# Performance work log

Measured on AMD Instinct MI355X. Metric: run time of the kernel, lower is better.

Reference implementation:

```python
import jax, jax.numpy as jnp
import numpy as np

BATCH, INPUT_SIZE, NUM_UNITS = 64, 256, 768
UNFOLDS = 6

def setup_inputs() -> dict:
    key = jax.random.key(0)
    ks = jax.random.split(key, 12)
    F, H = INPUT_SIZE, NUM_UNITS
    inputs = jax.random.normal(ks[0], (BATCH, F), dtype=jnp.float32)
    state = jax.random.normal(ks[1], (BATCH, H), dtype=jnp.float32)
    sensory_mu = jax.random.uniform(ks[2], (F, H), dtype=jnp.float32) * 0.5 + 0.3
    sensory_sigma = jax.random.uniform(ks[3], (F, H), dtype=jnp.float32) * 5.0 + 3.0
    sensory_W = jax.random.uniform(ks[4], (F, H), dtype=jnp.float32, minval=0.01, maxval=1.0)
    sensory_erev = (2.0 * jax.random.randint(ks[5], (F, H), 0, 2) - 1.0).astype(jnp.float32)
    mu = jax.random.uniform(ks[6], (H, H), dtype=jnp.float32) * 0.5 + 0.3
    sigma = jax.random.uniform(ks[7], (H, H), dtype=jnp.float32) * 5.0 + 3.0
    W = jax.random.uniform(ks[8], (H, H), dtype=jnp.float32, minval=0.01, maxval=1.0)
    erev = (2.0 * jax.random.randint(ks[9], (H, H), 0, 2) - 1.0).astype(jnp.float32)
    vleak = jax.random.uniform(ks[10], (H,), dtype=jnp.float32) * 0.4 - 0.2
    gleak = jnp.ones((H,), dtype=jnp.float32)          # gleak_init_min == gleak_init_max == 1
    cm_t = jnp.full((H,), 0.5, dtype=jnp.float32)      # cm_init_min == cm_init_max == 0.5
    input_w = jnp.ones((F,), dtype=jnp.float32)        # Affine mapping weight (ones)
    input_b = jnp.zeros((F,), dtype=jnp.float32)       # Affine mapping bias (zeros)
    return dict(inputs=inputs, state=state, input_w=input_w, input_b=input_b,
                sensory_mu=sensory_mu, sensory_sigma=sensory_sigma,
                sensory_W=sensory_W, sensory_erev=sensory_erev,
                mu=mu, sigma=sigma, W=W, erev=erev,
                vleak=vleak, gleak=gleak, cm_t=cm_t)

def reference(inputs, state, input_w, input_b, sensory_mu, sensory_sigma,
              sensory_W, sensory_erev, mu, sigma, W, erev, vleak, gleak, cm_t):
    x = inputs * input_w + input_b                                   # (B, F)
    # sensory pathway: (B, F, H) broadcast sigmoid, reduced over F
    s_act = sensory_W * jax.nn.sigmoid(sensory_sigma * (x[:, :, None] - sensory_mu))
    w_num_sensory = jnp.sum(s_act * sensory_erev, axis=1)            # (B, H)
    w_den_sensory = jnp.sum(s_act, axis=1)                           # (B, H)

    def step(v_pre, _):
        act = W * jax.nn.sigmoid(sigma * (v_pre[:, :, None] - mu))   # (B, H_pre, H_post)
        w_num = jnp.sum(act * erev, axis=1) + w_num_sensory          # (B, H)
        w_den = jnp.sum(act, axis=1) + w_den_sensory                 # (B, H)
        numerator = cm_t * v_pre + gleak * vleak + w_num
        denominator = cm_t + gleak + w_den
        return numerator / denominator, None

    v_pre, _ = jax.lax.scan(step, state, None, length=UNFOLDS)
    return (v_pre, v_pre)  # (outputs, next_state)
```

## Files before the change

### kernel.cpp

```cpp
#include <hip/hip_runtime.h>


constexpr int B_ = 64;
constexpr int F_ = 256;
constexpr int H_ = 768;
constexpr int UNFOLDS_ = 6;

constexpr int BB  = 4;
constexpr int JB  = 32;
constexpr int NSL = 8;
constexpr int NBLK = 384;
constexpr int ISL = H_ / NSL;
constexpr int FSL = F_ / NSL;

__device__ __forceinline__ void block_map(int blk, int& j0, int& b0) {
    int xcd = blk & 7;
    int kk  = blk >> 3;
    j0 = xcd * 96 + (kk % 3) * JB;
    b0 = (kk / 3) * BB;
}

__global__ __launch_bounds__(256) void sensory_k(
    const float* __restrict__ inputs, const float* __restrict__ iw,
    const float* __restrict__ ib,
    const float* __restrict__ smu, const float* __restrict__ ssig,
    const float* __restrict__ sW, const float* __restrict__ serev,
    float* __restrict__ sens_num, float* __restrict__ sens_den)
{
    int j0, b0;
    block_map(blockIdx.x, j0, b0);
    const int tid = threadIdx.x;
    const int jl = tid & (JB - 1), sl = tid / JB;
    const int j = j0 + jl;

    __shared__ float xs[BB][F_];
    __shared__ float red[2][NSL][BB][JB];

    for (int idx = tid; idx < BB * F_; idx += 256) {
        int b = idx >> 8, f = idx & (F_ - 1);
        xs[b][f] = fmaf(inputs[(b0 + b) * F_ + f], iw[f], ib[f]);
    }
    __syncthreads();

    const float L2E = 1.44269504088896f;
    float num[BB] = {0.f, 0.f, 0.f, 0.f}, den[BB] = {0.f, 0.f, 0.f, 0.f};
    const int fbase = sl * FSL;

    int idx0 = fbase * H_ + j;
    float sg = ssig[idx0], m = smu[idx0], w = sW[idx0], e = serev[idx0];
    for (int ff = 0; ff < FSL; ++ff) {
        float sgc = sg, mc = m, wc = w, ec = e;
        if (ff + 1 < FSL) {
            int idx = (fbase + ff + 1) * H_ + j;
            sg = ssig[idx]; m = smu[idx]; w = sW[idx]; e = serev[idx];
        }
        float sg2 = sgc * L2E;
        float c   = sg2 * mc;
        float we  = wc * ec;
#pragma unroll
        for (int k = 0; k < BB; ++k) {
            float t  = fmaf(-sg2, xs[k][fbase + ff], c);
            float ex = __builtin_amdgcn_exp2f(t);
            float s  = __builtin_amdgcn_rcpf(1.0f + ex);
            den[k] = fmaf(wc, s, den[k]);
            num[k] = fmaf(we, s, num[k]);
        }
    }
#pragma unroll
    for (int k = 0; k < BB; ++k) {
        red[0][sl][k][jl] = num[k];
        red[1][sl][k][jl] = den[k];
    }
    __syncthreads();

    if (tid < BB * JB) {
        int k = tid / JB, l = tid & (JB - 1);
        float n = 0.f, d = 0.f;
#pragma unroll
        for (int s = 0; s < NSL; ++s) { n += red[0][s][k][l]; d += red[1][s][k][l]; }
        int o = (b0 + k) * H_ + j0 + l;
        sens_num[o] = n;
        sens_den[o] = d;
    }
}

__global__ __launch_bounds__(256) void step_k(
    const float* __restrict__ v_in,
    const float* __restrict__ mu, const float* __restrict__ sigma,
    const float* __restrict__ W, const float* __restrict__ erev,
    const float* __restrict__ sens_num, const float* __restrict__ sens_den,
    const float* __restrict__ vleak, const float* __restrict__ gleak,
    const float* __restrict__ cm,
    float* __restrict__ v_out,
    float* __restrict__ out0, float* __restrict__ out1, int write_out)
{
    int j0, b0;
    block_map(blockIdx.x, j0, b0);
    const int tid = threadIdx.x;
    const int jl = tid & (JB - 1), sl = tid / JB;
    const int j = j0 + jl;

    __shared__ float vs[BB][H_];
    __shared__ float red[2][NSL][BB][JB];

    for (int idx = tid; idx < BB * H_; idx += 256) {
        int b = idx / H_, i = idx % H_;
        vs[b][i] = v_in[(b0 + b) * H_ + i];
    }
    __syncthreads();

    const float L2E = 1.44269504088896f;
    float num[BB] = {0.f, 0.f, 0.f, 0.f}, den[BB] = {0.f, 0.f, 0.f, 0.f};
    const int ibase = sl * ISL;

    int idx0 = ibase * H_ + j;
    float sg = sigma[idx0], m = mu[idx0], w = W[idx0], e = erev[idx0];
    for (int ii = 0; ii < ISL; ++ii) {
        float sgc = sg, mc = m, wc = w, ec = e;
        if (ii + 1 < ISL) {
            int idx = (ibase + ii + 1) * H_ + j;
            sg = sigma[idx]; m = mu[idx]; w = W[idx]; e = erev[idx];
        }
        float sg2 = sgc * L2E;
        float c   = sg2 * mc;
        float we  = wc * ec;
#pragma unroll
        for (int k = 0; k < BB; ++k) {
            float t  = fmaf(-sg2, vs[k][ibase + ii], c);
            float ex = __builtin_amdgcn_exp2f(t);
            float s  = __builtin_amdgcn_rcpf(1.0f + ex);
            den[k] = fmaf(wc, s, den[k]);
            num[k] = fmaf(we, s, num[k]);
        }
    }
#pragma unroll
    for (int k = 0; k < BB; ++k) {
        red[0][sl][k][jl] = num[k];
        red[1][sl][k][jl] = den[k];
    }
    __syncthreads();

    if (tid < BB * JB) {
        int k = tid / JB, l = tid & (JB - 1);
        int jj = j0 + l;
        float n = 0.f, d = 0.f;
#pragma unroll
        for (int s = 0; s < NSL; ++s) { n += red[0][s][k][l]; d += red[1][s][k][l]; }
        int o = (b0 + k) * H_ + jj;
        n += sens_num[o];
        d += sens_den[o];
        float g = gleak[jj];
        float numer = fmaf(cm[jj], vs[k][jj], fmaf(g, vleak[jj], n));
        float denom = cm[jj] + g + d;
        float vn = numer / denom;
        v_out[o] = vn;
        if (write_out) { out0[o] = vn; out1[o] = vn; }
    }
}

extern "C" void kernel_launch(void* const* d_in, const int* in_sizes, int n_in,
                              void* d_out, int out_size, void* d_ws, size_t ws_size,
                              hipStream_t stream) {
    const float* inputs = (const float*)d_in[0];
    const float* state  = (const float*)d_in[1];
    const float* iw     = (const float*)d_in[2];
    const float* ib     = (const float*)d_in[3];
    const float* smu    = (const float*)d_in[4];
    const float* ssig   = (const float*)d_in[5];
    const float* sW     = (const float*)d_in[6];
    const float* serev  = (const float*)d_in[7];
    const float* mu     = (const float*)d_in[8];
    const float* sigma  = (const float*)d_in[9];
    const float* W      = (const float*)d_in[10];
    const float* erev   = (const float*)d_in[11];
    const float* vleak  = (const float*)d_in[12];
    const float* gleak  = (const float*)d_in[13];
    const float* cm     = (const float*)d_in[14];
    float* out = (float*)d_out;

    float* ws = (float*)d_ws;
    float* sens_num = ws;
    float* sens_den = sens_num + B_ * H_;
    float* v0       = sens_den + B_ * H_;
    float* v1       = v0 + B_ * H_;

    sensory_k<<<NBLK, 256, 0, stream>>>(inputs, iw, ib, smu, ssig, sW, serev,
                                        sens_num, sens_den);

    const float* vin = state;
    for (int t = 0; t < UNFOLDS_; ++t) {
        float* vout = (t & 1) ? v1 : v0;
        int last = (t == UNFOLDS_ - 1);
        step_k<<<NBLK, 256, 0, stream>>>(vin, mu, sigma, W, erev,
                                         sens_num, sens_den, vleak, gleak, cm,
                                         vout, out, out + B_ * H_, last);
        vin = vout;
    }
}
```

Baseline: 237.3 us.

## Prepack transposed float4 parameters and split steps into partial and finalize kernels

A prep kernel transposes the sigma, mu, W and erev matrices into a per-output float4 layout holding the precomputed sigmoid coefficients and W*erev, and writes a transposed copy of the inputs. Each step then becomes a partial-sum kernel in which a wave's lanes map to the 64 batch rows, so each lane does a packed vector load of the shared parameters; the sensory pathway is merged into the first step's launch. A separate finalize kernel sums the 8 slices and applies the update. The goal is to stop re-fetching and recomputing parameter-derived values for every batch block and to get vectorized, batch-wide reuse, at the cost of a larger workspace (partial buffers), twice as many launches, and extra global traffic for the partial sums.

```diff
diff --git a/kernel.cpp b/kernel.cpp
--- a/kernel.cpp
+++ b/kernel.cpp
@@ -6,156 +6,198 @@
 constexpr int H_ = 768;
 constexpr int UNFOLDS_ = 6;
 
-constexpr int BB  = 4;
-constexpr int JB  = 32;
-constexpr int NSL = 8;
-constexpr int NBLK = 384;
-constexpr int ISL = H_ / NSL;
-constexpr int FSL = F_ / NSL;
-
-__device__ __forceinline__ void block_map(int blk, int& j0, int& b0) {
-    int xcd = blk & 7;
-    int kk  = blk >> 3;
-    j0 = xcd * 96 + (kk % 3) * JB;
-    b0 = (kk / 3) * BB;
-}
-
-__global__ __launch_bounds__(256) void sensory_k(
+constexpr int NS  = 8;
+constexpr int ISL = H_ / NS;
+constexpr int FSL = F_ / NS;
+constexpr int JG  = 96;
+constexpr int STEP_BLOCKS = JG * NS;
+constexpr int SENS_BLOCKS = JG * NS;
+constexpr int FIN_BLOCKS  = (B_ * H_) / 256;
+constexpr int TILE_STEP = (H_ / 32) * (H_ / 32);
+constexpr int TILE_SENS = (F_ / 32) * (H_ / 32);
+
+__global__ __launch_bounds__(256) void prep_k(
+    const float* __restrict__ sigma, const float* __restrict__ mu,
+    const float* __restrict__ W, const float* __restrict__ erev,
+    const float* __restrict__ ssig, const float* __restrict__ smu,
+    const float* __restrict__ sW, const float* __restrict__ serev,
     const float* __restrict__ inputs, const float* __restrict__ iw,
     const float* __restrict__ ib,
-    const float* __restrict__ smu, const float* __restrict__ ssig,
-    const float* __restrict__ sW, const float* __restrict__ serev,
-    float* __restrict__ sens_num, float* __restrict__ sens_den)
+    float4* __restrict__ pk_step,
+    float4* __restrict__ pk_sens,
+    float* __restrict__ xT)
 {
-    int j0, b0;
-    block_map(blockIdx.x, j0, b0);
     const int tid = threadIdx.x;
-    const int jl = tid & (JB - 1), sl = tid / JB;
-    const int j = j0 + jl;
-
-    __shared__ float xs[BB][F_];
-    __shared__ float red[2][NSL][BB][JB];
-
-    for (int idx = tid; idx < BB * F_; idx += 256) {
-        int b = idx >> 8, f = idx & (F_ - 1);
-        xs[b][f] = fmaf(inputs[(b0 + b) * F_ + f], iw[f], ib[f]);
-    }
-    __syncthreads();
-
     const float L2E = 1.44269504088896f;
-    float num[BB] = {0.f, 0.f, 0.f, 0.f}, den[BB] = {0.f, 0.f, 0.f, 0.f};
-    const int fbase = sl * FSL;
-
-    int idx0 = fbase * H_ + j;
-    float sg = ssig[idx0], m = smu[idx0], w = sW[idx0], e = serev[idx0];
-    for (int ff = 0; ff < FSL; ++ff) {
-        float sgc = sg, mc = m, wc = w, ec = e;
-        if (ff + 1 < FSL) {
-            int idx = (fbase + ff + 1) * H_ + j;
-            sg = ssig[idx]; m = smu[idx]; w = sW[idx]; e = serev[idx];
-        }
-        float sg2 = sgc * L2E;
-        float c   = sg2 * mc;
-        float we  = wc * ec;
+    int blk = blockIdx.x;
+
+    if (blk < TILE_STEP + TILE_SENS) {
+        const bool sens = blk >= TILE_STEP;
+        if (sens) blk -= TILE_STEP;
+        const int ti = blk / 24, tj = blk % 24;
+        const int i0 = ti * 32, j0 = tj * 32;
+        const float* A0 = sens ? ssig : sigma;
+        const float* A1 = sens ? smu : mu;
+        const float* A2 = sens ? sW : W;
+        const float* A3 = sens ? serev : erev;
+        float4* out = sens ? pk_sens : pk_step;
+        const int ILEN = sens ? F_ : H_;
+
+        __shared__ float tsg[32][33], tmu[32][33], tw[32][33], te[32][33];
+        const int col = tid & 31;
 #pragma unroll
-        for (int k = 0; k < BB; ++k) {
-            float t  = fmaf(-sg2, xs[k][fbase + ff], c);
-            float ex = __builtin_amdgcn_exp2f(t);
-            float s  = __builtin_amdgcn_rcpf(1.0f + ex);
-            den[k] = fmaf(wc, s, den[k]);
-            num[k] = fmaf(we, s, num[k]);
-        }
-    }
+        for (int k = 0; k < 4; ++k) {
+            int row = (tid >> 5) + k * 8;
+            int idx = (i0 + row) * H_ + j0 + col;
+            tsg[row][col] = A0[idx];
+            tmu[row][col] = A1[idx];
+            tw [row][col] = A2[idx];
+            te [row][col] = A3[idx];
+        }
+        __syncthreads();
 #pragma unroll
-    for (int k = 0; k < BB; ++k) {
-        red[0][sl][k][jl] = num[k];
-        red[1][sl][k][jl] = den[k];
-    }
-    __syncthreads();
-
-    if (tid < BB * JB) {
-        int k = tid / JB, l = tid & (JB - 1);
-        float n = 0.f, d = 0.f;
-#pragma unroll
-        for (int s = 0; s < NSL; ++s) { n += red[0][s][k][l]; d += red[1][s][k][l]; }
-        int o = (b0 + k) * H_ + j0 + l;
-        sens_num[o] = n;
-        sens_den[o] = d;
-    }
-}
-
-__global__ __launch_bounds__(256) void step_k(
-    const float* __restrict__ v_in,
-    const float* __restrict__ mu, const float* __restrict__ sigma,
-    const float* __restrict__ W, const float* __restrict__ erev,
-    const float* __restrict__ sens_num, const float* __restrict__ sens_den,
+        for (int k = 0; k < 4; ++k) {
+            int jj = (tid >> 5) + k * 8;
+            int ii = tid & 31;
+            float sg2 = tsg[ii][jj] * L2E;
+            float m   = tmu[ii][jj];
+            float w   = tw[ii][jj];
+            float e   = te[ii][jj];
+            float4 v;
+            v.x = sg2 * m;
+            v.y = -sg2;
+            v.z = w;
+            v.w = w * e;
+            out[(j0 + jj) * ILEN + (i0 + ii)] = v;
+        }
+    } else {
+        for (int e = tid; e < B_ * F_; e += 256) {
+            int f = e & (F_ - 1), b = e >> 8;
+            xT[f * B_ + b] = fmaf(inputs[b * F_ + f], iw[f], ib[f]);
+        }
+    }
+}
+
+__global__ __launch_bounds__(256) void part_k(
+    const float* __restrict__ v_src,
+    int first,
+    const float4* __restrict__ pk_step,
+    const float4* __restrict__ pk_sens,
+    const float* __restrict__ xT,
+    float* __restrict__ step_part,
+    float* __restrict__ sens_part)
+{
+    const int tid  = threadIdx.x;
+    const int lane = tid & 63;
+    const int wv   = __builtin_amdgcn_readfirstlane(tid >> 6);
+    __shared__ float vs[ISL * B_];
+
+    int sb = blockIdx.x;
+    if (sb < STEP_BLOCKS) {
+        const int jg = sb % JG, sl = sb / JG;
+        const int i0 = sl * ISL;
+        if (first) {
+            for (int e = tid; e < ISL * B_; e += 256) {
+                int ii = e >> 6, b = e & 63;
+                vs[ii * B_ + b] = v_src[b * H_ + i0 + ii];
+            }
+        } else {
+            for (int e = tid; e < ISL * B_; e += 256) {
+                int ii = e >> 6, b = e & 63;
+                vs[ii * B_ + b] = v_src[(i0 + ii) * B_ + b];
+            }
+        }
+        __syncthreads();
+
+        const int j = jg * 8 + wv * 2;
+        const float4* p0 = pk_step + j * H_ + i0;
+        const float4* p1 = p0 + H_;
+        float n0 = 0.f, d0 = 0.f, n1 = 0.f, d1 = 0.f;
+#pragma unroll 4
+        for (int ii = 0; ii < ISL; ++ii) {
+            float v  = vs[ii * B_ + lane];
+            float4 a = p0[ii];
+            float4 b4 = p1[ii];
+            float t0 = fmaf(a.y, v, a.x);
+            float t1 = fmaf(b4.y, v, b4.x);
+            float s0 = __builtin_amdgcn_rcpf(1.0f + __builtin_amdgcn_exp2f(t0));
+            float s1 = __builtin_amdgcn_rcpf(1.0f + __builtin_amdgcn_exp2f(t1));
+            d0 = fmaf(a.z,  s0, d0);
+            n0 = fmaf(a.w,  s0, n0);
+            d1 = fmaf(b4.z, s1, d1);
+            n1 = fmaf(b4.w, s1, n1);
+        }
+        float* pn = step_part + ((sl * 2 + 0) * H_) * B_;
+        float* pd = step_part + ((sl * 2 + 1) * H_) * B_;
+        pn[j * B_ + lane]       = n0;
+        pd[j * B_ + lane]       = d0;
+        pn[(j + 1) * B_ + lane] = n1;
+        pd[(j + 1) * B_ + lane] = d1;
+    } else {
+        const int s = sb - STEP_BLOCKS;
+        const int jg = s % JG, sl = s / JG;
+        const int f0 = sl * FSL;
+        for (int e = tid; e < FSL * B_; e += 256) {
+            int ff = e >> 6, b = e & 63;
+            vs[ff * B_ + b] = xT[(f0 + ff) * B_ + b];
+        }
+        __syncthreads();
+
+        const int j = jg * 8 + wv * 2;
+        const float4* p0 = pk_sens + j * F_ + f0;
+        const float4* p1 = p0 + F_;
+        float n0 = 0.f, d0 = 0.f, n1 = 0.f, d1 = 0.f;
+#pragma unroll 4
+        for (int ff = 0; ff < FSL; ++ff) {
+            float v  = vs[ff * B_ + lane];
+            float4 a = p0[ff];
+            float4 b4 = p1[ff];
+            float t0 = fmaf(a.y, v, a.x);
+            float t1 = fmaf(b4.y, v, b4.x);
+            float s0 = __builtin_amdgcn_rcpf(1.0f + __builtin_amdgcn_exp2f(t0));
+            float s1 = __builtin_amdgcn_rcpf(1.0f + __builtin_amdgcn_exp2f(t1));
+            d0 = fmaf(a.z,  s0, d0);
+            n0 = fmaf(a.w,  s0, n0);
+            d1 = fmaf(b4.z, s1, d1);
+            n1 = fmaf(b4.w, s1, n1);
+        }
+        float* pn = sens_part + ((sl * 2 + 0) * H_) * B_;
+        float* pd = sens_part + ((sl * 2 + 1) * H_) * B_;
+        pn[j * B_ + lane]       = n0;
+        pd[j * B_ + lane]       = d0;
+        pn[(j + 1) * B_ + lane] = n1;
+        pd[(j + 1) * B_ + lane] = d1;
+    }
+}
+
+__global__ __launch_bounds__(256) void fin_k(
+    const float* __restrict__ v_prev,
+    int first,
+    const float* __restrict__ step_part,
+    const float* __restrict__ sens_part,
     const float* __restrict__ vleak, const float* __restrict__ gleak,
     const float* __restrict__ cm,
-    float* __restrict__ v_out,
-    float* __restrict__ out0, float* __restrict__ out1, int write_out)
+    float* __restrict__ vT_out,
+    float* __restrict__ out0, float* __restrict__ out1, int last)
 {
-    int j0, b0;
-    block_map(blockIdx.x, j0, b0);
-    const int tid = threadIdx.x;
-    const int jl = tid & (JB - 1), sl = tid / JB;
-    const int j = j0 + jl;
-
-    __shared__ float vs[BB][H_];
-    __shared__ float red[2][NSL][BB][JB];
-
-    for (int idx = tid; idx < BB * H_; idx += 256) {
-        int b = idx / H_, i = idx % H_;
-        vs[b][i] = v_in[(b0 + b) * H_ + i];
-    }
-    __syncthreads();
-
-    const float L2E = 1.44269504088896f;
-    float num[BB] = {0.f, 0.f, 0.f, 0.f}, den[BB] = {0.f, 0.f, 0.f, 0.f};
-    const int ibase = sl * ISL;
-
-    int idx0 = ibase * H_ + j;
-    float sg = sigma[idx0], m = mu[idx0], w = W[idx0], e = erev[idx0];
-    for (int ii = 0; ii < ISL; ++ii) {
-        float sgc = sg, mc = m, wc = w, ec = e;
-        if (ii + 1 < ISL) {
-            int idx = (ibase + ii + 1) * H_ + j;
-            sg = sigma[idx]; m = mu[idx]; w = W[idx]; e = erev[idx];
-        }
-        float sg2 = sgc * L2E;
-        float c   = sg2 * mc;
-        float we  = wc * ec;
+    const int e = blockIdx.x * 256 + threadIdx.x;
+    const int b = e & 63, h = e >> 6;
+
+    float n = 0.f, d = 0.f;
 #pragma unroll
-        for (int k = 0; k < BB; ++k) {
-            float t  = fmaf(-sg2, vs[k][ibase + ii], c);
-            float ex = __builtin_amdgcn_exp2f(t);
-            float s  = __builtin_amdgcn_rcpf(1.0f + ex);
-            den[k] = fmaf(wc, s, den[k]);
-            num[k] = fmaf(we, s, num[k]);
-        }
-    }
-#pragma unroll
-    for (int k = 0; k < BB; ++k) {
-        red[0][sl][k][jl] = num[k];
-        red[1][sl][k][jl] = den[k];
-    }
-    __syncthreads();
-
-    if (tid < BB * JB) {
-        int k = tid / JB, l = tid & (JB - 1);
-        int jj = j0 + l;
-        float n = 0.f, d = 0.f;
-#pragma unroll
-        for (int s = 0; s < NSL; ++s) { n += red[0][s][k][l]; d += red[1][s][k][l]; }
-        int o = (b0 + k) * H_ + jj;
-        n += sens_num[o];
-        d += sens_den[o];
-        float g = gleak[jj];
-        float numer = fmaf(cm[jj], vs[k][jj], fmaf(g, vleak[jj], n));
-        float denom = cm[jj] + g + d;
-        float vn = numer / denom;
-        v_out[o] = vn;
-        if (write_out) { out0[o] = vn; out1[o] = vn; }
-    }
+    for (int sl = 0; sl < NS; ++sl) {
+        n += step_part[((sl * 2 + 0) * H_ + h) * B_ + b];
+        d += step_part[((sl * 2 + 1) * H_ + h) * B_ + b];
+        n += sens_part[((sl * 2 + 0) * H_ + h) * B_ + b];
+        d += sens_part[((sl * 2 + 1) * H_ + h) * B_ + b];
+    }
+    float vp = first ? v_prev[b * H_ + h] : v_prev[h * B_ + b];
+    float g  = gleak[h];
+    float numer = fmaf(cm[h], vp, fmaf(g, vleak[h], n));
+    float denom = cm[h] + g + d;
+    float vn = numer / denom;
+    vT_out[h * B_ + b] = vn;
+    if (last) { out0[b * H_ + h] = vn; out1[b * H_ + h] = vn; }
 }
 
 extern "C" void kernel_launch(void* const* d_in, const int* in_sizes, int n_in,
@@ -179,21 +221,28 @@
     float* out = (float*)d_out;
 
     float* ws = (float*)d_ws;
-    float* sens_num = ws;
-    float* sens_den = sens_num + B_ * H_;
-    float* v0       = sens_den + B_ * H_;
-    float* v1       = v0 + B_ * H_;
-
-    sensory_k<<<NBLK, 256, 0, stream>>>(inputs, iw, ib, smu, ssig, sW, serev,
-                                        sens_num, sens_den);
-
-    const float* vin = state;
+    float4* pk_step = (float4*)ws;
+    float4* pk_sens = pk_step + H_ * H_;
+    float*  xT      = (float*)(pk_sens + H_ * F_);
+    float*  step_part = xT + F_ * B_;
+    float*  sens_part = step_part + NS * 2 * H_ * B_;
+    float*  vT0       = sens_part + NS * 2 * H_ * B_;
+    float*  vT1       = vT0 + H_ * B_;
+
+    prep_k<<<TILE_STEP + TILE_SENS + 1, 256, 0, stream>>>(
+        sigma, mu, W, erev, ssig, smu, sW, serev, inputs, iw, ib,
+        pk_step, pk_sens, xT);
+
     for (int t = 0; t < UNFOLDS_; ++t) {
-        float* vout = (t & 1) ? v1 : v0;
-        int last = (t == UNFOLDS_ - 1);
-        step_k<<<NBLK, 256, 0, stream>>>(vin, mu, sigma, W, erev,
-                                         sens_num, sens_den, vleak, gleak, cm,
-                                         vout, out, out + B_ * H_, last);
-        vin = vout;
-    }
-}
+        const int first = (t == 0);
+        const int last  = (t == UNFOLDS_ - 1);
+        const float* vsrc = first ? state : ((t & 1) ? vT0 : vT1);
+        float* vdst = (t & 1) ? vT1 : vT0;
+        int nblk = first ? (STEP_BLOCKS + SENS_BLOCKS) : STEP_BLOCKS;
+        part_k<<<nblk, 256, 0, stream>>>(vsrc, first, pk_step, pk_sens, xT,
+                                         step_part, sens_part);
+        fin_k<<<FIN_BLOCKS, 256, 0, stream>>>(vsrc, first, step_part, sens_part,
+                                              vleak, gleak, cm, vdst,
+                                              out, out + B_ * H_, last);
+    }
+}
```

Result: faster. 213.1 us (-10.2%).
